# Kernel optimization log

Measured on AMD Instinct MI355X. Metric: run time of the kernel, lower is better.

The kernel has to match this reference:

```python
import jax, jax.numpy as jnp
import numpy as np

DIM = 512
BATCH = 4096
STEPS = 30
GOVERNOR_RANK = 321
LAMBDA_0 = 15.045
RANK_EPS = 1e-5


def setup_inputs() -> dict:
    key = jax.random.key(0)
    kx, kw = jax.random.split(key)
    x = jax.random.normal(kx, (BATCH, DIM), dtype=jnp.float32)
    # nn.Linear(dim, dim) with weight ~ N(0, (1.2/sqrt(dim))^2), bias = 0.01
    std = 1.2 / float(np.sqrt(DIM))
    W = jax.random.normal(kw, (DIM, DIM), dtype=jnp.float32) * std
    b = jnp.full((DIM,), 0.01, dtype=jnp.float32)
    return {"x": x, "W": W, "b": b}


def reference(x, W, b):
    # is_governed = governor_rank < 1e6 -> True, so the amplify branch is dead code.
    norm_factor = float(np.sqrt(BATCH * DIM))
    k = min(BATCH, DIM)  # number of singular values from thin SVD
    idx = jnp.arange(k)

    def step(h, _):
        h = h @ W.T + b  # [B, D]
        U, S, Vh = jnp.linalg.svd(h, full_matrices=False)  # U:[B,k] S:[k] Vh:[k,D]
        current_rank = jnp.sum(S > RANK_EPS)
        trunc = current_rank > GOVERNOR_RANK
        S = jnp.where(trunc & (idx >= GOVERNOR_RANK), 0.0, S)
        l1_sings = jnp.sum(S) / norm_factor  # recorded BEFORE rescale, as in torch
        scale = jnp.where(l1_sings > LAMBDA_0,
                          LAMBDA_0 * norm_factor / jnp.sum(S), 1.0)
        h = (U * (S * scale)) @ Vh  # reconstruct U diag(S) Vh
        return h, l1_sings

    _, activations = jax.lax.scan(step, x, None, length=STEPS)
    return activations  # [STEPS] l1 singular-value sums, matching the returned list
```

## Files before the change

### kernel.cpp

```cpp
#include <hip/hip_runtime.h>
#include <math.h>

#define DIM 512
#define BATCH 4096
#define NSTEPS 30
#define KEEP 321

#define S_BETA 0
#define S_SCALE 1
#define S_VTV 4
#define S_SC 5

#define TDG 32
#define MTAIL 96

__device__ __forceinline__ double wred(double v) {
#pragma unroll
  for (int o = 32; o > 0; o >>= 1) v += __shfl_down(v, (unsigned)o, 64);
  return v;
}

__device__ __forceinline__ void stg(double* p, double v) {
  __hip_atomic_store(p, v, __ATOMIC_RELAXED, __HIP_MEMORY_SCOPE_AGENT);
}
__device__ __forceinline__ double ldg_(const double* p) {
  return __hip_atomic_load(p, __ATOMIC_RELAXED, __HIP_MEMORY_SCOPE_AGENT);
}

__device__ __forceinline__ void gbar2(unsigned* __restrict__ flags, unsigned& gen) {
  gen++;
  const unsigned target = gen;
  __syncthreads();
  if (threadIdx.x == 0) {
    __threadfence();
    __hip_atomic_store(flags + (size_t)blockIdx.x * 32, target, __ATOMIC_RELAXED, __HIP_MEMORY_SCOPE_AGENT);
  }
  if (threadIdx.x < 64) {
    bool ok = ((int)threadIdx.x >= TDG);
    while (!__all(ok)) {
      if (!ok) {
        unsigned v = __hip_atomic_load(flags + (size_t)threadIdx.x * 32, __ATOMIC_RELAXED, __HIP_MEMORY_SCOPE_AGENT);
        ok = (v >= target);
      }
    }
    __threadfence();
  }
  __syncthreads();
}

__device__ __forceinline__ void gbarf(unsigned* __restrict__ flags, unsigned& gen) {
  gen++;
  const unsigned target = gen;
  __syncthreads();
  if (threadIdx.x == 0) {
    __hip_atomic_store(flags + (size_t)blockIdx.x * 32, target, __ATOMIC_RELAXED, __HIP_MEMORY_SCOPE_AGENT);
  }
  if (threadIdx.x < 64) {
    bool ok = ((int)threadIdx.x >= TDG);
    while (!__all(ok)) {
      if (!ok) {
        unsigned v = __hip_atomic_load(flags + (size_t)threadIdx.x * 32, __ATOMIC_RELAXED, __HIP_MEMORY_SCOPE_AGENT);
        ok = (v >= target);
      }
    }
    asm volatile("" ::: "memory");
  }
  __syncthreads();
}


__global__ __launch_bounds__(256) void k_cast(const float* __restrict__ W, const float* __restrict__ b,
                                              double* __restrict__ Wd, double* __restrict__ bd,
                                              unsigned* __restrict__ cflags) {
  int idx = blockIdx.x * 256 + threadIdx.x;
  if (idx < DIM * DIM) Wd[idx] = (double)W[idx];
  if (idx < DIM) bd[idx] = (double)b[idx];
  if (blockIdx.x == 0) {
    for (int i = threadIdx.x; i < 1024; i += 256) cflags[i] = 0;
  }
}

__global__ __launch_bounds__(512) void k_colsum(const float* __restrict__ x, double* __restrict__ mvec) {
  int j = threadIdx.x;
  double s = 0.0;
  for (int r = 0; r < BATCH; ++r) s += (double)x[(size_t)r * DIM + j];
  mvec[j] = s;
}

__global__ __launch_bounds__(256) void k_xtx(const float* __restrict__ x, double* __restrict__ Gx) {
  __shared__ double As[16][65];
  __shared__ double Bs[16][65];
  const int tid = threadIdx.x;
  const int tx = tid & 15, ty = tid >> 4;
  const int bi = blockIdx.y * 64, bj = blockIdx.x * 64;
  const int lr = tid >> 4, lc4 = (tid & 15) * 4;
  double acc[4][4] = {};
  for (int r0 = 0; r0 < BATCH; r0 += 16) {
#pragma unroll
    for (int q = 0; q < 4; ++q) {
      As[lr][lc4 + q] = (double)x[(size_t)(r0 + lr) * DIM + bi + lc4 + q];
      Bs[lr][lc4 + q] = (double)x[(size_t)(r0 + lr) * DIM + bj + lc4 + q];
    }
    __syncthreads();
#pragma unroll
    for (int rr = 0; rr < 16; ++rr) {
      double a[4], bb[4];
#pragma unroll
      for (int u = 0; u < 4; ++u) a[u] = As[rr][ty * 4 + u];
#pragma unroll
      for (int v = 0; v < 4; ++v) bb[v] = Bs[rr][tx * 4 + v];
#pragma unroll
      for (int u = 0; u < 4; ++u)
#pragma unroll
        for (int v = 0; v < 4; ++v) acc[u][v] += a[u] * bb[v];
    }
    __syncthreads();
  }
#pragma unroll
  for (int u = 0; u < 4; ++u)
#pragma unroll
    for (int v = 0; v < 4; ++v) Gx[(size_t)(bi + ty * 4 + u) * DIM + bj + tx * 4 + v] = acc[u][v];
}

__global__ __launch_bounds__(256) void k_chol_mw(const double* __restrict__ G, double* __restrict__ R,
                                                 unsigned* __restrict__ flags) {
  __shared__ double Lr[16][512];
  __shared__ double rowk[512];
  const int tid = threadIdx.x, lane = tid & 63, wid = tid >> 6;
  const int g = blockIdx.x;
  unsigned gen = 0;
  for (int s = 0; s < 16; ++s) {
    const int i = s * 32 + g;
    for (int j = tid; j < DIM; j += 256) Lr[s][j] = G[(size_t)i * DIM + j];
  }
  __syncthreads();
  for (int k = 0; k < DIM; ++k) {
    if ((k & 31) == g) {
      const int s = k >> 5;
      double dkk = Lr[s][k];
      double sq = sqrt(fmax(dkk, 1e-280));
      double inv = 1.0 / sq;
      for (int j = tid; j < DIM; j += 256) {
        double v;
        if (j < k) v = 0.0;
        else if (j == k) v = sq;
        else v = Lr[s][j] * inv;
        stg(&R[(size_t)k * DIM + j], v);
      }
    }
    gbarf(flags, gen);
    for (int j = k + tid; j < DIM; j += 256) rowk[j] = ldg_(&R[(size_t)k * DIM + j]);
    __syncthreads();
    for (int s = wid; s < 16; s += 4) {
      const int i = s * 32 + g;
      if (i <= k) continue;
      const double rki = rowk[i];
      for (int j = i + lane; j < DIM; j += 64) Lr[s][j] -= rki * rowk[j];
    }
    __syncthreads();
  }
}

__global__ __launch_bounds__(64) void k_solvec0(const double* __restrict__ R, const double* __restrict__ mvec,
                                                double* __restrict__ c0) {
  const int lane = threadIdx.x;
  double rhs[8], cs[8];
#pragma unroll
  for (int r = 0; r < 8; ++r) rhs[r] = mvec[lane + 64 * r];
#pragma unroll
  for (int r = 0; r < 8; ++r) cs[r] = 0.0;
  for (int i = 0; i < DIM; ++i) {
    int owner = i & 63, ri = i >> 6;
    double ci = 0.0;
    if (lane == owner) {
      ci = rhs[ri] / R[(size_t)i * DIM + i];
      cs[ri] = ci;
    }
    ci = __shfl(ci, owner, 64);
    const double* row = R + (size_t)i * DIM;
#pragma unroll
    for (int r = 0; r < 8; ++r) {
      int j = lane + 64 * r;
      if (j > i) rhs[r] -= ci * row[j];
    }
  }
#pragma unroll
  for (int r = 0; r < 8; ++r) c0[lane + 64 * r] = cs[r];
}


__global__ __launch_bounds__(512) void k_prep(const double* __restrict__ cstv, const double* __restrict__ bd, int r,
                                              double* __restrict__ tvec, double* __restrict__ Mm,
                                              double* __restrict__ scal, unsigned* __restrict__ tflags) {
  __shared__ double redb[8];
  __shared__ double bc[1];
  const int tid = threadIdx.x, lane = tid & 63, wid = tid >> 6;
  for (int i = tid; i < 1024; i += 512) tflags[i] = 0;
  double p = 0.0;
  for (int i = tid; i < r; i += 512) {
    double c = cstv[i];
    p += c * c;
    tvec[i] = c;
  }
  p = wred(p);
  if (lane == 0) redb[wid] = p;
  __syncthreads();
  if (tid == 0) {
    double s = 0;
    for (int q = 0; q < 8; ++q) s += redb[q];
    double beta = sqrt(fmax(4096.0 - s, 1e-20));
    tvec[r] = beta;
    scal[S_BETA] = beta;
    bc[0] = beta;
  }
  __syncthreads();
  double beta = bc[0];
  for (int j = tid; j < DIM; j += 512) Mm[(size_t)r * DIM + j] = beta * bd[j];
}

__global__ __launch_bounds__(256) void k_gemm_nt(const double* __restrict__ A, const double* __restrict__ B,
                                                 double* __restrict__ C, int M, int N, int Kd, int lda, int ldb, int ldc,
                                                 const double* __restrict__ ur, const double* __restrict__ vr) {
  __shared__ double As[16][65];
  __shared__ double Bs[16][65];
  const int tid = threadIdx.x;
  const int tx = tid & 15, ty = tid >> 4;
  const int bi = blockIdx.y * 64, bj = blockIdx.x * 64;
  const int li = tid >> 2, lk = (tid & 3) * 4;
  double acc[4][4] = {};
  for (int k0 = 0; k0 < Kd; k0 += 16) {
    int gi = bi + li;
    bool oa = (gi < M);
    const double* pa = A + (size_t)(oa ? gi : 0) * lda + k0 + lk;
    int gj = bj + li;
    bool ob = (gj < N);
    const double* pb = B + (size_t)(ob ? gj : 0) * ldb + k0 + lk;
#pragma unroll
    for (int q = 0; q < 4; ++q) {
      int gk = k0 + lk + q;
      As[lk + q][li] = (oa && gk < Kd) ? pa[q] : 0.0;
      Bs[lk + q][li] = (ob && gk < Kd) ? pb[q] : 0.0;
    }
    __syncthreads();
#pragma unroll
    for (int kk = 0; kk < 16; ++kk) {
      double a[4], bb[4];
#pragma unroll
      for (int u = 0; u < 4; ++u) a[u] = As[kk][ty * 4 + u];
#pragma unroll
      for (int v = 0; v < 4; ++v) bb[v] = Bs[kk][tx * 4 + v];
#pragma unroll
      for (int u = 0; u < 4; ++u)
#pragma unroll
        for (int v = 0; v < 4; ++v) acc[u][v] += a[u] * bb[v];
    }
    __syncthreads();
  }
#pragma unroll
  for (int u = 0; u < 4; ++u) {
    int gi = bi + ty * 4 + u;
    if (gi >= M) continue;
#pragma unroll
    for (int v = 0; v < 4; ++v) {
      int gj = bj + tx * 4 + v;
      if (gj >= N) continue;
      double val = acc[u][v];
      if (ur) val += ur[gi] * vr[gj];
      C[(size_t)gi * ldc + gj] = val;
    }
  }
}

__global__ __launch_bounds__(256) void k_syrk(const double* __restrict__ M, double* __restrict__ C, int n, int Kd,
                                              int ld, int ldc) {
  __shared__ double As[16][65];
  __shared__ double Bs[16][65];
  int bid = blockIdx.x;
  int by = 0;
  while ((by + 1) * (by + 2) / 2 <= bid) by++;
  int bx = bid - by * (by + 1) / 2;
  const int tid = threadIdx.x;
  const int tx = tid & 15, ty = tid >> 4;
  const int bi = by * 64, bj = bx * 64;
  const int li = tid >> 2, lk = (tid & 3) * 4;
  double acc[4][4] = {};
  for (int k0 = 0; k0 < Kd; k0 += 16) {
    int gi = bi + li;
    bool oa = (gi < n);
    const double* pa = M + (size_t)(oa ? gi : 0) * ld + k0 + lk;
    int gj = bj + li;
    bool ob = (gj < n);
    const double* pb = M + (size_t)(ob ? gj : 0) * ld + k0 + lk;
#pragma unroll
    for (int q = 0; q < 4; ++q) {
      As[lk + q][li] = oa ? pa[q] : 0.0;
      Bs[lk + q][li] = ob ? pb[q] : 0.0;
    }
    __syncthreads();
#pragma unroll
    for (int kk = 0; kk < 16; ++kk) {
      double a[4], bb[4];
#pragma unroll
      for (int u = 0; u < 4; ++u) a[u] = As[kk][ty * 4 + u];
#pragma unroll
      for (int v = 0; v < 4; ++v) bb[v] = Bs[kk][tx * 4 + v];
#pragma unroll
      for (int u = 0; u < 4; ++u)
#pragma unroll
        for (int v = 0; v < 4; ++v) acc[u][v] += a[u] * bb[v];
    }
    __syncthreads();
  }
#pragma unroll
  for (int u = 0; u < 4; ++u) {
    int gi = bi + ty * 4 + u;
    if (gi >= n) continue;
#pragma unroll
    for (int v = 0; v < 4; ++v) {
      int gj = bj + tx * 4 + v;
      if (gj >= n) continue;
      double val = acc[u][v];
      C[(size_t)gi * ldc + gj] = val;
      if (by > bx) C[(size_t)gj * ldc + gi] = val;
    }
  }
}

__global__ __launch_bounds__(256) void k_tridiag_mw(double* __restrict__ A, int n, double* __restrict__ d,
                                                    double* __restrict__ e, double* __restrict__ tau,
                                                    double* __restrict__ Vrow, double* __restrict__ pvec,
                                                    double* __restrict__ orow, double* __restrict__ vtpp,
                                                    unsigned* __restrict__ flags) {
  __shared__ double vsh[520];
  __shared__ double wsh[520];
  __shared__ double xsh[520];
  __shared__ double redb[4];
  __shared__ double redb2[4];
  __shared__ double bc[1];
  const int tid = threadIdx.x, lane = tid & 63, wid = tid >> 6;
  const int g = blockIdx.x;
  unsigned gen = 0;
  const int ktail = n - 1 - MTAIL;
  double dval = A[0];
  for (int i = tid; i < n - 1; i += 256) xsh[i] = A[1 + i];
  __syncthreads();
  for (int k = 0; k < ktail; ++k) {
    const int m = n - 1 - k;
    const int par = k & 1;
    double* __restrict__ pv = pvec + par * 520;
    double* __restrict__ orw = orow + par * 520;
    double* __restrict__ vt = vtpp + par * 32;
    double part = 0.0;
    for (int i = tid; i < m; i += 256) {
      double xi = xsh[i];
      part += xi * xi;
    }
    part = wred(part);
    if (lane == 0) redb[wid] = part;
    __syncthreads();
    double s2 = redb[0] + redb[1] + redb[2] + redb[3];
    double x0 = xsh[0];
    double tk, v0, alpha;
    if (s2 < 1e-260) {
      tk = 0.0;
      v0 = 0.0;
      alpha = x0;
    } else {
      double sig = sqrt(s2);
      alpha = (x0 >= 0.0) ? -sig : sig;
      v0 = x0 - alpha;
      double vn2 = s2 - x0 * x0 + v0 * v0;
      tk = 2.0 / vn2;
    }
    for (int i = tid; i < m; i += 256) vsh[i] = (i == 0) ? v0 : xsh[i];
    __syncthreads();
    if (g == 0 && tid == 0) {
      d[k] = dval;
      e[k] = alpha;
      tau[k] = tk;
    }
    {
      double* __restrict__ Vr = Vrow + (size_t)k * n;
      for (int i = g * 256 + tid; i < m; i += TDG * 256) Vr[i] = vsh[i];
    }
    if (((k + 1) & (TDG - 1)) == g) {
      const double* __restrict__ rk1 = A + (size_t)(k + 1) * n + (k + 1);
      for (int j = tid; j < m; j += 256) stg(&orw[j], rk1[j]);
    }
    const int rem = (k + 1) & (TDG - 1);
    const int r0 = (k + 1) + ((g - rem + TDG) & (TDG - 1));
    double vtp = 0.0;
    for (int r = r0 + wid * TDG; r < n; r += 4 * TDG) {
      const int i = r - (k + 1);
      const double* __restrict__ row = A + (size_t)r * n + (k + 1);
      double acc = 0.0;
      for (int j = lane; j < m; j += 64) acc += row[j] * vsh[j];
      acc = wred(acc);
      if (lane == 0) {
        double pi = tk * acc;
        stg(&pv[i], pi);
        vtp += vsh[i] * pi;
      }
    }
    if (lane == 0) redb2[wid] = vtp;
    __syncthreads();
    if (tid == 0) stg(&vt[g], redb2[0] + redb2[1] + redb2[2] + redb2[3]);
    gbarf(flags, gen);
    if (wid == 0) {
      double vv = (lane < TDG) ? ldg_(&vt[lane]) : 0.0;
      vv = wred(vv);
      if (lane == 0) bc[0] = vv;
    }
    __syncthreads();
    const double K0 = 0.5 * tk * bc[0];
    const double vv0 = vsh[0];
    const double w0 = ldg_(&pv[0]) - K0 * vv0;
    for (int i = tid; i < m; i += 256) {
      double w = ldg_(&pv[i]) - K0 * vsh[i];
      wsh[i] = w;
      if (i >= 1) xsh[i - 1] = ldg_(&orw[i]) - vsh[i] * w0 - w * vv0;
    }
    if (tid == 0) dval = ldg_(&orw[0]) - 2.0 * vv0 * w0;
    __syncthreads();
    for (int r = r0 + wid * TDG; r < n; r += 4 * TDG) {
      const int i = r - (k + 1);
      const double vi = vsh[i], wi = wsh[i];
      double* __restrict__ row = A + (size_t)r * n + (k + 1);
      for (int j = lane; j < m; j += 64) row[j] -= vi * wsh[j] + wi * vsh[j];
    }
    __syncthreads();
  }
  gbar2(flags, gen);
  if (g != 0) return;
  for (int k = ktail; k <= n - 3; ++k) {
    const int m = n - 1 - k;
    double part = 0.0;
    for (int i = tid; i < m; i += 256) {
      double xi = xsh[i];
      vsh[i] = xi;
      part += xi * xi;
    }
    part = wred(part);
    if (lane == 0) redb[wid] = part;
    __syncthreads();
    double s2 = redb[0] + redb[1] + redb[2] + redb[3];
    double x0 = vsh[0];
    double tk, v0, alpha;
    if (s2 < 1e-260) {
      tk = 0.0;
      v0 = 0.0;
      alpha = x0;
    } else {
      double sig = sqrt(s2);
      alpha = (x0 >= 0.0) ? -sig : sig;
      v0 = x0 - alpha;
      double vn2 = s2 - x0 * x0 + v0 * v0;
      tk = 2.0 / vn2;
    }
    __syncthreads();
    if (tid == 0) {
      vsh[0] = v0;
      d[k] = A[(size_t)k * n + k];
      e[k] = alpha;
      tau[k] = tk;
    }
    __syncthreads();
    double* __restrict__ Vr = Vrow + (size_t)k * n;
    for (int i = tid; i < m; i += 256) Vr[i] = vsh[i];
    double vtp = 0.0;
    for (int i = wid; i < m; i += 4) {
      const double* __restrict__ row = A + (size_t)(k + 1 + i) * n + (k + 1);
      double acc = 0.0;
      for (int j = lane; j < m; j += 64) acc += row[j] * vsh[j];
      acc = wred(acc);
      if (lane == 0) {
        double pi = tk * acc;
        wsh[i] = pi;
        vtp += vsh[i] * pi;
      }
    }
    if (lane == 0) redb2[wid] = vtp;
    __syncthreads();
    const double K0 = 0.5 * tk * (redb2[0] + redb2[1] + redb2[2] + redb2[3]);
    for (int i = wid; i < m; i += 4) {
      const double vi = vsh[i];
      const double ci = wsh[i] - 2.0 * K0 * vsh[i];
      double* __restrict__ row = A + (size_t)(k + 1 + i) * n + (k + 1);
      for (int j = lane; j < m; j += 64) {
        double nv = row[j] - (vi * wsh[j] + ci * vsh[j]);
        row[j] = nv;
        if (j == 0 && i >= 1) xsh[i - 1] = nv;
      }
    }
    __syncthreads();
  }
  if (tid == 0) {
    d[n - 2] = A[(size_t)(n - 2) * n + (n - 2)];
    e[n - 2] = A[(size_t)(n - 1) * n + (n - 2)];
    d[n - 1] = A[(size_t)(n - 1) * n + (n - 1)];
  }
}

__global__ __launch_bounds__(64) void k_bisect_ms(const double* __restrict__ d, const double* __restrict__ e, int n,
                                                  double* __restrict__ lam) {
  __shared__ double ds[520];
  __shared__ double e2s[520];
  const int lane = threadIdx.x;
  const int ev = blockIdx.x;
  for (int i = lane; i < n; i += 64) {
    ds[i] = d[i];
    e2s[i] = (i >= 1) ? e[i - 1] * e[i - 1] : 0.0;
  }
  __syncthreads();
  double glo = 1e300, ghi = -1e300, me2 = 0.0;
  for (int i = lane; i < n; i += 64) {
    double ea = (i >= 1) ? sqrt(e2s[i]) : 0.0;
    double eb = (i < n - 1) ? sqrt(e2s[i + 1]) : 0.0;
    glo = fmin(glo, ds[i] - ea - eb);
    ghi = fmax(ghi, ds[i] + ea + eb);
    me2 = fmax(me2, e2s[i]);
  }
#pragma unroll
  for (int o = 32; o > 0; o >>= 1) {
    glo = fmin(glo, __shfl_down(glo, (unsigned)o, 64));
    ghi = fmax(ghi, __shfl_down(ghi, (unsigned)o, 64));
    me2 = fmax(me2, __shfl_down(me2, (unsigned)o, 64));
  }
  glo = __shfl(glo, 0, 64);
  ghi = __shfl(ghi, 0, 64);
  me2 = __shfl(me2, 0, 64);
  double span = ghi - glo;
  double lo = glo - 1e-3 * span - 1e-30;
  double hi = ghi + 1e-3 * span + 1e-30;
  const double pivmin = fmax(me2 * 2.220446049250313e-16, 1e-280);
  for (int r = 0; r < 7; ++r) {
    const double x = lo + (hi - lo) * ((double)(lane + 1) * (1.0 / 65.0));
    int cnt = 0;
    double q = ds[0] - x;
    if (q < 0.0) cnt++;
    for (int i = 1; i < n; ++i) {
      double t = q;
      if (fabs(t) < pivmin) t = (t < 0.0) ? -pivmin : pivmin;
      q = (ds[i] - x) - e2s[i] / t;
      if (q < 0.0) cnt++;
    }
    unsigned long long mask = __ballot(cnt <= ev);
    int pc = (int)__popcll(mask);
    double nlo = (pc > 0) ? __shfl(x, pc - 1, 64) : lo;
    double nhi = (pc < 64) ? __shfl(x, pc, 64) : hi;
    lo = nlo;
    hi = nhi;
  }
  if (lane == 0) lam[ev] = 0.5 * (lo + hi);
}

__global__ __launch_bounds__(64) void k_specsum(const double* __restrict__ lam, int n, int keep_start, int step,
                                                float* __restrict__ out, double* __restrict__ scal) {
  if (threadIdx.x == 0) {
    int cnt = 0;
    double st = 0.0, sa = 0.0;
    for (int i = 0; i < n; ++i) {
      double l = lam[i];
      double s = (l > 0.0) ? sqrt(l) : 0.0;
      if (s > 1e-5) cnt++;
      sa += s;
      if (i >= keep_start) st += s;
    }
    bool trunc = (cnt > 321);
    double ssum = trunc ? st : sa;
    const double NORMF = 1448.1546878700494;
    double l1 = ssum / NORMF;
    out[step] = (float)l1;
    scal[S_SCALE] = (l1 > 15.045) ? (15.045 / l1) : 1.0;
  }
}

__global__ __launch_bounds__(512) void k_eigvec(const double* __restrict__ Vrow, int n, const double* __restrict__ d,
                                                const double* __restrict__ e, const double* __restrict__ tau,
                                                const double* __restrict__ lam, const double* __restrict__ Mm,
                                                const double* __restrict__ tvec, double* __restrict__ scal,
                                                double* __restrict__ vhh, double* __restrict__ g) {
  __shared__ double zs[384];
  __shared__ double cps[384];
  __shared__ double dsh[384];
  __shared__ double esh[384];
  __shared__ double tsh[384];
  __shared__ double tvsh[384];
  __shared__ double bc[2];
  const int tid = threadIdx.x;
  for (int i = tid; i < n; i += 512) {
    dsh[i] = d[i];
    esh[i] = e[i];
    tsh[i] = tau[i];
    tvsh[i] = tvec[i];
  }
  __syncthreads();
  if (tid == 0) {
    double lmax = fabs(lam[n - 1]);
    double sh = lam[0] - (1e-12 * lmax + 1e-280);
    double me2 = 0.0;
    for (int i = 1; i < n; ++i) {
      double t = esh[i - 1];
      me2 = fmax(me2, t * t);
    }
    double pivmin = fmax(me2 * 2.220446049250313e-16, 1e-280);
    unsigned s = 0xB5297A4Du;
    for (int i = 0; i < n; ++i) {
      s = s * 1664525u + 1013904223u;
      zs[i] = 0.75 + (double)(s >> 8) * (0.5 / 16777216.0);
    }
    for (int it = 0; it < 3; ++it) {
      double den = dsh[0] - sh;
      if (fabs(den) < pivmin) den = (den < 0) ? -pivmin : pivmin;
      cps[0] = esh[0] / den;
      zs[0] = zs[0] / den;
      for (int i = 1; i < n; ++i) {
        den = (dsh[i] - sh) - esh[i - 1] * cps[i - 1];
        if (fabs(den) < pivmin) den = (den < 0) ? -pivmin : pivmin;
        cps[i] = (i < n - 1) ? esh[i] / den : 0.0;
        zs[i] = (zs[i] - esh[i - 1] * zs[i - 1]) / den;
      }
      for (int i = n - 2; i >= 0; --i) zs[i] -= cps[i] * zs[i + 1];
      double nn = 0;
      for (int i = 0; i < n; ++i) nn += zs[i] * zs[i];
      double inv = 1.0 / sqrt(fmax(nn, 1e-300));
      for (int i = 0; i < n; ++i) zs[i] *= inv;
    }
  }
  __syncthreads();
  if (tid < 64) {
    double z[6];
#pragma unroll
    for (int r = 0; r < 6; ++r) {
      int j = tid + 64 * r;
      z[r] = (j < n) ? zs[j] : 0.0;
    }
    for (int k = n - 3; k >= 0; --k) {
      const double tk = tsh[k];
      const double* __restrict__ vr = Vrow + (size_t)k * n;
      double vv[6];
#pragma unroll
      for (int r = 0; r < 6; ++r) {
        int j = tid + 64 * r;
        vv[r] = (j >= k + 1 && j < n) ? vr[j - k - 1] : 0.0;
      }
      double p = 0.0;
#pragma unroll
      for (int r = 0; r < 6; ++r) p += vv[r] * z[r];
      p = wred(p);
      p = __shfl(p, 0, 64);
      double tp = tk * p;
#pragma unroll
      for (int r = 0; r < 6; ++r) z[r] -= tp * vv[r];
    }
    double nn = 0.0;
#pragma unroll
    for (int r = 0; r < 6; ++r) nn += z[r] * z[r];
    nn = wred(nn);
    nn = __shfl(nn, 0, 64);
    double inv = 1.0 / sqrt(fmax(nn, 1e-300));
#pragma unroll
    for (int r = 0; r < 6; ++r) {
      int j = tid + 64 * r;
      if (j < n) zs[j] = z[r] * inv;
    }
  }
  __syncthreads();
  if (tid == 0) {
    double wl = zs[n - 1];
    double sg = (wl >= 0.0) ? 1.0 : -1.0;
    double coef = 1.0 / (1.0 + fabs(wl));
    zs[n - 1] = wl + sg;
    scal[S_VTV] = 2.0 + 2.0 * fabs(wl);
    bc[0] = coef;
    double sc = 0.0;
    for (int i = 0; i < n; ++i) sc += zs[i] * tvsh[i];
    scal[S_SC] = sc * coef;
  }
  __syncthreads();
  const double coef = bc[0];
  {
    double acc = 0.0;
    for (int i = 0; i < n; ++i) acc += zs[i] * Mm[(size_t)i * DIM + tid];
    g[tid] = coef * acc;
  }
  for (int i = tid; i < n; i += 512) vhh[i] = zs[i];
}

__global__ __launch_bounds__(512) void k_ii_multi(const double* __restrict__ d, const double* __restrict__ e,
                                                  const double* __restrict__ lam, int n, int keep_start,
                                                  double* __restrict__ Uk, double* __restrict__ cp) {
  const int tid = threadIdx.x, lane = tid & 63, wid = tid >> 6;
  __shared__ double redb[8];
  __shared__ double bc[1];
  if (tid < KEEP) {
    int j = tid;
    double lj = lam[keep_start + j];
    double me2 = 0.0;
    for (int i = 1; i < n; ++i) {
      double t = e[i - 1];
      me2 = fmax(me2, t * t);
    }
    double pivmin = fmax(me2 * 2.220446049250313e-16, 1e-280);
    unsigned s = 0x9E3779B9u * (unsigned)(j + 13);
    for (int i = 0; i < n; ++i) {
      s = s * 1664525u + 1013904223u;
      Uk[(size_t)i * KEEP + j] = 0.5 + (double)(s >> 8) * (1.0 / 16777216.0);
    }
    for (int it = 0; it < 3; ++it) {
      double den = d[0] - lj;
      if (fabs(den) < pivmin) den = (den < 0.0) ? -pivmin : pivmin;
      double cprev = e[0] / den;
      cp[0 * KEEP + j] = cprev;
      double zprev = Uk[0 * KEEP + j] / den;
      Uk[0 * KEEP + j] = zprev;
      for (int i = 1; i < n; ++i) {
        den = (d[i] - lj) - e[i - 1] * cprev;
        if (fabs(den) < pivmin) den = (den < 0.0) ? -pivmin : pivmin;
        double ci = (i < n - 1) ? e[i] / den : 0.0;
        cp[(size_t)i * KEEP + j] = ci;
        double zi = (Uk[(size_t)i * KEEP + j] - e[i - 1] * zprev) / den;
        Uk[(size_t)i * KEEP + j] = zi;
        zprev = zi;
        cprev = ci;
      }
      double zn = Uk[(size_t)(n - 1) * KEEP + j];
      for (int i = n - 2; i >= 0; --i) {
        zn = Uk[(size_t)i * KEEP + j] - cp[(size_t)i * KEEP + j] * zn;
        Uk[(size_t)i * KEEP + j] = zn;
      }
      double nn = 0;
      for (int i = 0; i < n; ++i) {
        double z = Uk[(size_t)i * KEEP + j];
        nn += z * z;
      }
      double inv = 1.0 / sqrt(fmax(nn, 1e-300));
      for (int i = 0; i < n; ++i) Uk[(size_t)i * KEEP + j] *= inv;
    }
  }
  __syncthreads();
  for (int jj = 1; jj < KEEP; ++jj) {
    double l1v = lam[keep_start + jj], l0v = lam[keep_start + jj - 1];
    bool close = (l1v - l0v) < 1e-7 * (fabs(l1v) + 1e-280);
    if (!close) continue;
    double p = 0;
    for (int i = tid; i < n; i += 512) p += Uk[(size_t)i * KEEP + jj] * Uk[(size_t)i * KEEP + jj - 1];
    p = wred(p);
    if (lane == 0) redb[wid] = p;
    __syncthreads();
    if (tid == 0) {
      double s2 = 0;
      for (int q = 0; q < 8; ++q) s2 += redb[q];
      bc[0] = s2;
    }
    __syncthreads();
    double dot = bc[0];
    for (int i = tid; i < n; i += 512) Uk[(size_t)i * KEEP + jj] -= dot * Uk[(size_t)i * KEEP + jj - 1];
    __syncthreads();
    p = 0;
    for (int i = tid; i < n; i += 512) {
      double z = Uk[(size_t)i * KEEP + jj];
      p += z * z;
    }
    p = wred(p);
    if (lane == 0) redb[wid] = p;
    __syncthreads();
    if (tid == 0) {
      double s2 = 0;
      for (int q = 0; q < 8; ++q) s2 += redb[q];
      bc[0] = 1.0 / sqrt(fmax(s2, 1e-300));
    }
    __syncthreads();
    double inv = bc[0];
    for (int i = tid; i < n; i += 512) Uk[(size_t)i * KEEP + jj] *= inv;
    __syncthreads();
  }
}

__global__ __launch_bounds__(64) void k_hhapply_multi(const double* __restrict__ Vrow, const double* __restrict__ tau,
                                                      int n, double* __restrict__ Uk) {
  const int j = blockIdx.x;
  const int lane = threadIdx.x;
  for (int k = n - 3; k >= 0; --k) {
    double tk = tau[k];
    if (tk == 0.0) continue;
    int m = n - 1 - k;
    const double* __restrict__ vr = Vrow + (size_t)k * n;
    double p = 0.0;
    for (int i = lane; i < m; i += 64) p += vr[i] * Uk[(size_t)(k + 1 + i) * KEEP + j];
    p = wred(p);
    p = __shfl(p, 0, 64);
    double tp = tk * p;
    for (int i = lane; i < m; i += 64) Uk[(size_t)(k + 1 + i) * KEEP + j] -= tp * vr[i];
  }
  double nn = 0.0;
  for (int i = lane; i < n; i += 64) {
    double z = Uk[(size_t)i * KEEP + j];
    nn += z * z;
  }
  nn = wred(nn);
  nn = __shfl(nn, 0, 64);
  double inv = 1.0 / sqrt(fmax(nn, 1e-300));
  for (int i = lane; i < n; i += 64) Uk[(size_t)i * KEEP + j] *= inv;
}

__global__ __launch_bounds__(256) void k_gemm_tn(const double* __restrict__ A, const double* __restrict__ B,
                                                 double* __restrict__ C, int M, int N, int Kd, int lda, int ldb, int ldc,
                                                 const double* __restrict__ scal) {
  __shared__ double As[16][65];
  __shared__ double Bs[16][65];
  const int tid = threadIdx.x;
  const int tx = tid & 15, ty = tid >> 4;
  const int bi = blockIdx.y * 64, bj = blockIdx.x * 64;
  const int li = tid & 63, lq = tid >> 6;
  double acc[4][4] = {};
  for (int k0 = 0; k0 < Kd; k0 += 16) {
#pragma unroll
    for (int q = 0; q < 4; ++q) {
      int kk = lq + q * 4;
      int gk = k0 + kk;
      int gi = bi + li;
      int gj = bj + li;
      As[kk][li] = (gi < M && gk < Kd) ? A[(size_t)gk * lda + gi] : 0.0;
      Bs[kk][li] = (gj < N && gk < Kd) ? B[(size_t)gk * ldb + gj] : 0.0;
    }
    __syncthreads();
#pragma unroll
    for (int kk = 0; kk < 16; ++kk) {
      double a[4], bb[4];
#pragma unroll
      for (int u = 0; u < 4; ++u) a[u] = As[kk][ty * 4 + u];
#pragma unroll
      for (int v = 0; v < 4; ++v) bb[v] = Bs[kk][tx * 4 + v];
#pragma unroll
      for (int u = 0; u < 4; ++u)
#pragma unroll
        for (int v = 0; v < 4; ++v) acc[u][v] += a[u] * bb[v];
    }
    __syncthreads();
  }
  double s = scal[S_SCALE];
#pragma unroll
  for (int u = 0; u < 4; ++u) {
    int gi = bi + ty * 4 + u;
    if (gi >= M) continue;
#pragma unroll
    for (int v = 0; v < 4; ++v) {
      int gj = bj + tx * 4 + v;
      if (gj >= N) continue;
      C[(size_t)gi * ldc + gj] = s * acc[u][v];
    }
  }
}

__global__ __launch_bounds__(512) void k_gemv_tn(const double* __restrict__ Uk, const double* __restrict__ tvec,
                                                 double* __restrict__ cstv, int n) {
  int i = threadIdx.x;
  if (i < KEEP) {
    double acc = 0.0;
    for (int k = 0; k < n; ++k) acc += Uk[(size_t)k * KEEP + i] * tvec[k];
    cstv[i] = acc;
  }
}

__global__ __launch_bounds__(256) void k_hh_update(const double* __restrict__ Mm, const double* __restrict__ vhh,
                                                   const double* __restrict__ g, const double* __restrict__ scal,
                                                   const double* __restrict__ tvec, double* __restrict__ Cst,
                                                   double* __restrict__ cstv) {
  int idx = blockIdx.x * 256 + threadIdx.x;
  double scale = scal[S_SCALE];
  if (idx < KEEP * DIM) {
    int i = idx >> 9, j = idx & 511;
    Cst[(size_t)i * DIM + j] = scale * (Mm[(size_t)i * DIM + j] - vhh[i] * g[j]);
  }
  if (blockIdx.x == 0 && threadIdx.x < KEEP) {
    cstv[threadIdx.x] = tvec[threadIdx.x] - vhh[threadIdx.x] * scal[S_SC];
  }
}


extern "C" void kernel_launch(void* const* d_in, const int* in_sizes, int n_in, void* d_out, int out_size, void* d_ws,
                              size_t ws_size, hipStream_t stream) {
  (void)in_sizes;
  (void)n_in;
  (void)out_size;
  (void)ws_size;
  const float* x = (const float*)d_in[0];
  const float* W = (const float*)d_in[1];
  const float* b = (const float*)d_in[2];
  float* out = (float*)d_out;

  char* ws = (char*)d_ws;
  size_t off = 0;
  auto alloc = [&](size_t nelem) {
    size_t p = off;
    off += (nelem * 8 + 255) & ~(size_t)255;
    return (double*)(ws + p);
  };
  double* Wd = alloc(512 * 512);
  double* bd = alloc(512);
  double* mvec = alloc(512);
  double* Cst = alloc(512 * 512);
  double* cstv = alloc(520);
  double* tvec = alloc(520);
  double* Mm = alloc(513 * 512);
  double* AwGx = alloc(513 * 513);
  double* Gx = AwGx;
  double* Aw = AwGx;
  double* zcp = AwGx;
  double* Vrow = alloc(513 * 513);
  double* dT = alloc(520);
  double* eT = alloc(520);
  double* tauT = alloc(520);
  double* lam = alloc(520);
  double* vhh = alloc(520);
  double* gv = alloc(520);
  double* scal = alloc(32);
  double* Uk = alloc(513 * 321);
  double* pvec = alloc(1040);
  double* orow = alloc(1040);
  double* vtpp = alloc(64);
  unsigned* tflags = (unsigned*)alloc(512);
  unsigned* cflags = (unsigned*)alloc(512);

  k_cast<<<dim3((512 * 512 + 255) / 256), dim3(256), 0, stream>>>(W, b, Wd, bd, cflags);
  k_colsum<<<dim3(1), dim3(512), 0, stream>>>(x, mvec);
  k_xtx<<<dim3(8, 8), dim3(256), 0, stream>>>(x, Gx);
  k_chol_mw<<<dim3(TDG), dim3(256), 0, stream>>>(Gx, Cst, cflags);
  k_solvec0<<<dim3(1), dim3(64), 0, stream>>>(Cst, mvec, cstv);

  {
    const int r = 512, n = 513;
    k_prep<<<dim3(1), dim3(512), 0, stream>>>(cstv, bd, r, tvec, Mm, scal, tflags);
    k_gemm_nt<<<dim3(8, 8), dim3(256), 0, stream>>>(Cst, Wd, Mm, r, 512, 512, 512, 512, 512, cstv, bd);
    k_syrk<<<dim3(45), dim3(256), 0, stream>>>(Mm, Aw, n, 512, 512, n);
    k_tridiag_mw<<<dim3(TDG), dim3(256), 0, stream>>>(Aw, n, dT, eT, tauT, Vrow, pvec, orow, vtpp, tflags);
    k_bisect_ms<<<dim3(n), dim3(64), 0, stream>>>(dT, eT, n, lam);
    k_specsum<<<dim3(1), dim3(64), 0, stream>>>(lam, n, n - KEEP, 0, out, scal);
    k_ii_multi<<<dim3(1), dim3(512), 0, stream>>>(dT, eT, lam, n, n - KEEP, Uk, zcp);
    k_hhapply_multi<<<dim3(KEEP), dim3(64), 0, stream>>>(Vrow, tauT, n, Uk);
    k_gemm_tn<<<dim3(8, 6), dim3(256), 0, stream>>>(Uk, Mm, Cst, KEEP, 512, n, KEEP, 512, 512, scal);
    k_gemv_tn<<<dim3(1), dim3(512), 0, stream>>>(Uk, tvec, cstv, n);
  }

  for (int t = 1; t < NSTEPS; ++t) {
    const int r = KEEP, n = KEEP + 1;
    k_prep<<<dim3(1), dim3(512), 0, stream>>>(cstv, bd, r, tvec, Mm, scal, tflags);
    k_gemm_nt<<<dim3(8, 6), dim3(256), 0, stream>>>(Cst, Wd, Mm, r, 512, 512, 512, 512, 512, cstv, bd);
    k_syrk<<<dim3(21), dim3(256), 0, stream>>>(Mm, Aw, n, 512, 512, n);
    k_tridiag_mw<<<dim3(TDG), dim3(256), 0, stream>>>(Aw, n, dT, eT, tauT, Vrow, pvec, orow, vtpp, tflags);
    k_bisect_ms<<<dim3(n), dim3(64), 0, stream>>>(dT, eT, n, lam);
    k_specsum<<<dim3(1), dim3(64), 0, stream>>>(lam, n, 1, t, out, scal);
    k_eigvec<<<dim3(1), dim3(512), 0, stream>>>(Vrow, n, dT, eT, tauT, lam, Mm, tvec, scal, vhh, gv);
    k_hh_update<<<dim3((KEEP * DIM + 255) / 256), dim3(256), 0, stream>>>(Mm, vhh, gv, scal, tvec, Cst, cstv);
  }
}
```

Measured before the change: 106.4 ms.

## Keep tridiagonalization matrix rows resident in LDS across 8 workgroups

Adds a tridiagonal-reduction kernel for the 322x322 steady-state steps. It distributes matrix rows cyclically over 8 workgroups and keeps them in shared memory for the whole multi-workgroup phase, instead of streaming rows from global memory with 32 workgroups. Only the tail submatrix is written back to global memory for the single-workgroup finish. This removes global-memory traffic and shrinks the grid barrier to 8 participants. The cost is less parallelism per step and a large LDS footprint of about 106KB per workgroup.

After: 120.5 ms. +13.2%, slower.

```diff
diff --git a/kernel.cpp b/kernel.cpp
--- a/kernel.cpp
+++ b/kernel.cpp
@@ -14,6 +14,11 @@
 #define TDG 32
 #define MTAIL 96
 
+#define N2 322
+#define TD2 8
+#define ROWS2 41
+#define LDP (N2 + 2)
+
 __device__ __forceinline__ double wred(double v) {
 #pragma unroll
   for (int o = 32; o > 0; o >>= 1) v += __shfl_down(v, (unsigned)o, 64);
@@ -27,7 +32,7 @@
   return __hip_atomic_load(p, __ATOMIC_RELAXED, __HIP_MEMORY_SCOPE_AGENT);
 }
 
-__device__ __forceinline__ void gbar2(unsigned* __restrict__ flags, unsigned& gen) {
+__device__ __forceinline__ void gbar2(unsigned* __restrict__ flags, unsigned& gen, int nwg) {
   gen++;
   const unsigned target = gen;
   __syncthreads();
@@ -36,7 +41,7 @@
     __hip_atomic_store(flags + (size_t)blockIdx.x * 32, target, __ATOMIC_RELAXED, __HIP_MEMORY_SCOPE_AGENT);
   }
   if (threadIdx.x < 64) {
-    bool ok = ((int)threadIdx.x >= TDG);
+    bool ok = ((int)threadIdx.x >= nwg);
     while (!__all(ok)) {
       if (!ok) {
         unsigned v = __hip_atomic_load(flags + (size_t)threadIdx.x * 32, __ATOMIC_RELAXED, __HIP_MEMORY_SCOPE_AGENT);
@@ -48,7 +53,7 @@
   __syncthreads();
 }
 
-__device__ __forceinline__ void gbarf(unsigned* __restrict__ flags, unsigned& gen) {
+__device__ __forceinline__ void gbarf(unsigned* __restrict__ flags, unsigned& gen, int nwg) {
   gen++;
   const unsigned target = gen;
   __syncthreads();
@@ -56,7 +61,7 @@
     __hip_atomic_store(flags + (size_t)blockIdx.x * 32, target, __ATOMIC_RELAXED, __HIP_MEMORY_SCOPE_AGENT);
   }
   if (threadIdx.x < 64) {
-    bool ok = ((int)threadIdx.x >= TDG);
+    bool ok = ((int)threadIdx.x >= nwg);
     while (!__all(ok)) {
       if (!ok) {
         unsigned v = __hip_atomic_load(flags + (size_t)threadIdx.x * 32, __ATOMIC_RELAXED, __HIP_MEMORY_SCOPE_AGENT);
@@ -148,7 +153,7 @@
         stg(&R[(size_t)k * DIM + j], v);
       }
     }
-    gbarf(flags, gen);
+    gbarf(flags, gen, TDG);
     for (int j = k + tid; j < DIM; j += 256) rowk[j] = ldg_(&R[(size_t)k * DIM + j]);
     __syncthreads();
     for (int s = wid; s < 16; s += 4) {
@@ -405,7 +410,7 @@
     if (lane == 0) redb2[wid] = vtp;
     __syncthreads();
     if (tid == 0) stg(&vt[g], redb2[0] + redb2[1] + redb2[2] + redb2[3]);
-    gbarf(flags, gen);
+    gbarf(flags, gen, TDG);
     if (wid == 0) {
       double vv = (lane < TDG) ? ldg_(&vt[lane]) : 0.0;
       vv = wred(vv);
@@ -430,7 +435,7 @@
     }
     __syncthreads();
   }
-  gbar2(flags, gen);
+  gbar2(flags, gen, TDG);
   if (g != 0) return;
   for (int k = ktail; k <= n - 3; ++k) {
     const int m = n - 1 - k;
@@ -490,6 +495,193 @@
         double nv = row[j] - (vi * wsh[j] + ci * vsh[j]);
         row[j] = nv;
         if (j == 0 && i >= 1) xsh[i - 1] = nv;
+      }
+    }
+    __syncthreads();
+  }
+  if (tid == 0) {
+    d[n - 2] = A[(size_t)(n - 2) * n + (n - 2)];
+    e[n - 2] = A[(size_t)(n - 1) * n + (n - 2)];
+    d[n - 1] = A[(size_t)(n - 1) * n + (n - 1)];
+  }
+}
+
+__global__ __launch_bounds__(256) void k_tridiag_lds(double* __restrict__ A, double* __restrict__ d,
+                                                     double* __restrict__ e, double* __restrict__ tau,
+                                                     double* __restrict__ Vrow, double* __restrict__ pvec,
+                                                     double* __restrict__ orow, double* __restrict__ vtpp,
+                                                     unsigned* __restrict__ flags) {
+  const int n = N2;
+  __shared__ double Ald[ROWS2][LDP];
+  __shared__ double vg[LDP];
+  __shared__ double wg[LDP];
+  __shared__ double xg[LDP];
+  __shared__ double redb[4];
+  __shared__ double redb2[4];
+  __shared__ double bc[1];
+  const int tid = threadIdx.x, lane = tid & 63, wid = tid >> 6;
+  const int g = blockIdx.x;
+  unsigned gen = 0;
+  const int ktail = n - 1 - MTAIL;
+  for (int r = g; r < n; r += TD2) {
+    double* __restrict__ dst = Ald[r >> 3];
+    const double* __restrict__ src = A + (size_t)r * n;
+    for (int c = tid; c < n; c += 256) dst[c] = src[c];
+  }
+  double dval = A[0];
+  for (int c = 1 + tid; c < n; c += 256) xg[c] = A[c];
+  __syncthreads();
+
+  for (int k = 0; k < ktail; ++k) {
+    const int m = n - 1 - k;
+    const int par = k & 1;
+    double* __restrict__ pv = pvec + par * 520;
+    double* __restrict__ orw = orow + par * 520;
+    double* __restrict__ vt = vtpp + par * 32;
+    double part = 0.0;
+    for (int c = k + 1 + tid; c < n; c += 256) part += xg[c] * xg[c];
+    part = wred(part);
+    if (lane == 0) redb[wid] = part;
+    __syncthreads();
+    double s2 = redb[0] + redb[1] + redb[2] + redb[3];
+    double x0 = xg[k + 1];
+    double tk, v0, alpha;
+    if (s2 < 1e-260) {
+      tk = 0.0;
+      v0 = 0.0;
+      alpha = x0;
+    } else {
+      double sig = sqrt(s2);
+      alpha = (x0 >= 0.0) ? -sig : sig;
+      v0 = x0 - alpha;
+      double vn2 = s2 - x0 * x0 + v0 * v0;
+      tk = 2.0 / vn2;
+    }
+    for (int c = k + 1 + tid; c < n; c += 256) vg[c] = (c == k + 1) ? v0 : xg[c];
+    __syncthreads();
+    if (g == 0 && tid == 0) {
+      d[k] = dval;
+      e[k] = alpha;
+      tau[k] = tk;
+    }
+    {
+      double* __restrict__ Vr = Vrow + (size_t)k * n;
+      for (int i = g * 256 + tid; i < m; i += TD2 * 256) Vr[i] = vg[k + 1 + i];
+    }
+    if (((k + 1) % TD2) == g) {
+      const double* __restrict__ rk1 = Ald[(k + 1) >> 3];
+      for (int j = tid; j < m; j += 256) stg(&orw[j], rk1[k + 1 + j]);
+    }
+    const int rem = (k + 1) % TD2;
+    const int r0 = (k + 1) + ((g - rem + TD2) % TD2);
+    double vtp = 0.0;
+    for (int r = r0 + wid * TD2; r < n; r += 4 * TD2) {
+      const double* __restrict__ row = Ald[r >> 3];
+      double acc = 0.0;
+      for (int c = k + 1 + lane; c < n; c += 64) acc += row[c] * vg[c];
+      acc = wred(acc);
+      if (lane == 0) {
+        double pi = tk * acc;
+        stg(&pv[r - (k + 1)], pi);
+        vtp += vg[r] * pi;
+      }
+    }
+    if (lane == 0) redb2[wid] = vtp;
+    __syncthreads();
+    if (tid == 0) stg(&vt[g], redb2[0] + redb2[1] + redb2[2] + redb2[3]);
+    gbarf(flags, gen, TD2);
+    if (wid == 0) {
+      double vv = (lane < TD2) ? ldg_(&vt[lane]) : 0.0;
+      vv = wred(vv);
+      if (lane == 0) bc[0] = vv;
+    }
+    __syncthreads();
+    const double K0 = 0.5 * tk * bc[0];
+    const double vv0 = vg[k + 1];
+    const double w0 = ldg_(&pv[0]) - K0 * vv0;
+    for (int i = tid; i < m; i += 256) {
+      const int c = k + 1 + i;
+      double w = ldg_(&pv[i]) - K0 * vg[c];
+      wg[c] = w;
+      if (i >= 1) xg[c] = ldg_(&orw[i]) - vg[c] * w0 - w * vv0;
+    }
+    if (tid == 0) dval = ldg_(&orw[0]) - 2.0 * vv0 * w0;
+    __syncthreads();
+    for (int r = r0 + wid * TD2; r < n; r += 4 * TD2) {
+      const double vr = vg[r], wr = wg[r];
+      double* __restrict__ row = Ald[r >> 3];
+      for (int c = k + 1 + lane; c < n; c += 64) row[c] -= vr * wg[c] + wr * vg[c];
+    }
+    __syncthreads();
+  }
+  for (int r = g; r < n; r += TD2) {
+    if (r < ktail) continue;
+    const double* __restrict__ src = Ald[r >> 3];
+    double* __restrict__ dst = A + (size_t)r * n;
+    for (int c = ktail + tid; c < n; c += 256) dst[c] = src[c];
+  }
+  gbar2(flags, gen, TD2);
+  if (g != 0) return;
+  for (int k = ktail; k <= n - 3; ++k) {
+    const int m = n - 1 - k;
+    double part = 0.0;
+    for (int c = k + 1 + tid; c < n; c += 256) {
+      double xi = xg[c];
+      vg[c] = xi;
+      part += xi * xi;
+    }
+    part = wred(part);
+    if (lane == 0) redb[wid] = part;
+    __syncthreads();
+    double s2 = redb[0] + redb[1] + redb[2] + redb[3];
+    double x0 = vg[k + 1];
+    double tk, v0, alpha;
+    if (s2 < 1e-260) {
+      tk = 0.0;
+      v0 = 0.0;
+      alpha = x0;
+    } else {
+      double sig = sqrt(s2);
+      alpha = (x0 >= 0.0) ? -sig : sig;
+      v0 = x0 - alpha;
+      double vn2 = s2 - x0 * x0 + v0 * v0;
+      tk = 2.0 / vn2;
+    }
+    __syncthreads();
+    if (tid == 0) {
+      vg[k + 1] = v0;
+      d[k] = (k == ktail) ? dval : A[(size_t)k * n + k];
+      e[k] = alpha;
+      tau[k] = tk;
+    }
+    __syncthreads();
+    double* __restrict__ Vr = Vrow + (size_t)k * n;
+    for (int i = tid; i < m; i += 256) Vr[i] = vg[k + 1 + i];
+    double vtp = 0.0;
+    for (int i = wid; i < m; i += 4) {
+      const int r = k + 1 + i;
+      const double* __restrict__ row = A + (size_t)r * n;
+      double acc = 0.0;
+      for (int c = k + 1 + lane; c < n; c += 64) acc += row[c] * vg[c];
+      acc = wred(acc);
+      if (lane == 0) {
+        double pi = tk * acc;
+        wg[r] = pi;
+        vtp += vg[r] * pi;
+      }
+    }
+    if (lane == 0) redb2[wid] = vtp;
+    __syncthreads();
+    const double K0 = 0.5 * tk * (redb2[0] + redb2[1] + redb2[2] + redb2[3]);
+    for (int i = wid; i < m; i += 4) {
+      const int r = k + 1 + i;
+      const double vr = vg[r];
+      const double cr = wg[r] - 2.0 * K0 * vr;
+      double* __restrict__ row = A + (size_t)r * n;
+      for (int c = k + 1 + lane; c < n; c += 64) {
+        double nv = row[c] - (vr * wg[c] + cr * vg[c]);
+        row[c] = nv;
+        if (c == k + 1 && r >= k + 2) xg[r] = nv;
       }
     }
     __syncthreads();
@@ -948,7 +1140,7 @@
     k_prep<<<dim3(1), dim3(512), 0, stream>>>(cstv, bd, r, tvec, Mm, scal, tflags);
     k_gemm_nt<<<dim3(8, 6), dim3(256), 0, stream>>>(Cst, Wd, Mm, r, 512, 512, 512, 512, 512, cstv, bd);
     k_syrk<<<dim3(21), dim3(256), 0, stream>>>(Mm, Aw, n, 512, 512, n);
-    k_tridiag_mw<<<dim3(TDG), dim3(256), 0, stream>>>(Aw, n, dT, eT, tauT, Vrow, pvec, orow, vtpp, tflags);
+    k_tridiag_lds<<<dim3(TD2), dim3(256), 0, stream>>>(Aw, dT, eT, tauT, Vrow, pvec, orow, vtpp, tflags);
     k_bisect_ms<<<dim3(n), dim3(64), 0, stream>>>(dT, eT, n, lam);
     k_specsum<<<dim3(1), dim3(64), 0, stream>>>(lam, n, 1, t, out, scal);
     k_eigvec<<<dim3(1), dim3(512), 0, stream>>>(Vrow, n, dT, eT, tauT, lam, Mm, tvec, scal, vhh, gv);
```
